# Optimization experiments

Measured on AMD Instinct MI355X. Metric: run time of the kernel, lower is better.

## Reference

```python
import jax, jax.numpy as jnp
import numpy as np

BN_EPS = 1e-5


def setup_inputs() -> dict:
    key = jax.random.key(0)
    k1, k2 = jax.random.split(key)
    B, P, S, D = 8, 64, 256, 256
    x = jax.random.normal(k1, (B, P, S, D), dtype=jnp.float32)
    # kaiming_normal_ on (planes, S, S): std = sqrt(2 / fan_in), fan_in = S*S
    std = np.sqrt(2.0 / (S * S)).astype(np.float32)
    weights = jax.random.normal(k2, (P, S, S), dtype=jnp.float32) * std
    gamma = jnp.ones((P,), dtype=jnp.float32)
    beta = jnp.zeros((P,), dtype=jnp.float32)
    return {"x": x, "weights": weights, "gamma": gamma, "beta": beta}


def reference(x, weights, gamma, beta):
    # x: (B, P, S, D); weights: (P, S, S)
    D = x.shape[-1]
    inv_dim = 1.0 / jnp.sqrt(jnp.asarray(D, dtype=x.dtype))
    # scores: (B, P, S, S) = x @ x^T / sqrt(D)
    scores = jnp.einsum('bpsd,bptd->bpst', x, x) * inv_dim
    # weighted reduction over last axis -> (B, P, S, 1)
    red = jnp.sum(scores * weights[None], axis=-1, keepdims=True)
    y = x + red  # residual broadcast over D
    # BatchNorm2d in training mode: per-channel batch stats over (B, S, D)
    mean = jnp.mean(y, axis=(0, 2, 3), keepdims=True)
    var = jnp.var(y, axis=(0, 2, 3), keepdims=True)
    y_hat = (y - mean) * jax.lax.rsqrt(var + BN_EPS)
    return y_hat * gamma[None, :, None, None] + beta[None, :, None, None]
```

## Files before the change

kernel.cpp:

```cpp
#include <hip/hip_runtime.h>

typedef __attribute__((ext_vector_type(8))) short short8;
typedef __attribute__((ext_vector_type(4))) float f32x4;

#define NB 8
#define NP 64
#define NS 256
#define ND 256
#define LSTR 264

__device__ __forceinline__ unsigned short f2bf(float f) {
    unsigned int u = __float_as_uint(f);
    u = (u + 0x7FFFu + ((u >> 16) & 1u)) >> 16;
    return (unsigned short)u;
}

__global__ __launch_bounds__(256) void k0_wt(
    const float* __restrict__ w, float* __restrict__ wt)
{
    const int o  = blockIdx.x * 256 + threadIdx.x;
    const int c  = o & 15;
    const int jb = (o >> 4) & 3;
    const int ps = o >> 6;
    const float* row = w + (size_t)ps * NS + 64 * jb + c;
    f32x4 v;
    v.x = row[0]; v.y = row[16]; v.z = row[32]; v.w = row[48];
    reinterpret_cast<f32x4*>(wt)[o] = v;
}

__global__ __launch_bounds__(1024, 4) void k1_gemm_red(
    const float* __restrict__ x, const float* __restrict__ wt,
    float* __restrict__ red, float* __restrict__ Sx, float* __restrict__ Sxx)
{
    __shared__ unsigned short Xl[NS * LSTR];
    __shared__ float red_l[4][NS];

    const int t    = threadIdx.x;
    const int lane = t & 63;
    const int wv   = t >> 6;
    const int ib   = wv >> 2;
    const int jb   = wv & 3;
    const int p    = blockIdx.x & 63;
    const int b    = blockIdx.x >> 6;

    const float* xb      = x + (size_t)(b * NP + p) * (NS * ND);
    const size_t rowbase = (size_t)(b * NP + p) * NS;

    #pragma unroll 4
    for (int i = 0; i < 16; ++i) {
        const int row = 16 * i + wv;
        f32x4 v = *reinterpret_cast<const f32x4*>(xb + row * ND + 4 * lane);
        float a = (v.x + v.y) + (v.z + v.w);
        #pragma unroll
        for (int off = 1; off < 64; off <<= 1) a += __shfl_xor(a, off, 64);
        if (lane == 0) Sx[rowbase + row] = a;
        unsigned long long pk =
              (unsigned long long)f2bf(v.x)
            | ((unsigned long long)f2bf(v.y) << 16)
            | ((unsigned long long)f2bf(v.z) << 32)
            | ((unsigned long long)f2bf(v.w) << 48);
        *reinterpret_cast<unsigned long long*>(&Xl[row * LSTR + 4 * lane]) = pk;
    }
    __syncthreads();

    const int qd = lane >> 4;
    const int c  = lane & 15;

    f32x4 acc[4][4] = {};
    #pragma unroll 2
    for (int k0 = 0; k0 < ND; k0 += 32) {
        const int kof = k0 + qd * 8;
        short8 afr[4], bfr[4];
        #pragma unroll
        for (int i = 0; i < 4; ++i)
            afr[i] = *reinterpret_cast<const short8*>(
                &Xl[(64 * ib + 16 * i + c) * LSTR + kof]);
        #pragma unroll
        for (int j = 0; j < 4; ++j)
            bfr[j] = *reinterpret_cast<const short8*>(
                &Xl[(64 * jb + 16 * j + c) * LSTR + kof]);
        #pragma unroll
        for (int i = 0; i < 4; ++i)
            #pragma unroll
            for (int j = 0; j < 4; ++j)
                acc[i][j] = __builtin_amdgcn_mfma_f32_16x16x32_bf16(
                    afr[i], bfr[j], acc[i][j], 0, 0, 0);
    }

    if (ib == jb && qd == (c >> 2)) {
        #pragma unroll
        for (int i = 0; i < 4; ++i)
            Sxx[rowbase + 64 * ib + 16 * i + c] = acc[i][i][c & 3];
    }

    const float* wtp = wt + (size_t)p * (NS * NS);
    #pragma unroll
    for (int i = 0; i < 4; ++i) {
        #pragma unroll
        for (int r = 0; r < 4; ++r) {
            const int rl = 16 * i + 4 * qd + r;
            const f32x4 wv = *reinterpret_cast<const f32x4*>(
                wtp + (size_t)(64 * ib + rl) * NS + 64 * jb + 4 * c);
            float s = acc[i][0][r] * wv.x + acc[i][1][r] * wv.y
                    + acc[i][2][r] * wv.z + acc[i][3][r] * wv.w;
            #pragma unroll
            for (int off = 1; off < 16; off <<= 1)
                s += __shfl_xor(s, off, 64);
            if (c == 0) red_l[jb][64 * ib + rl] = s;
        }
    }
    __syncthreads();
    if (t < NS)
        red[rowbase + t] =
            (red_l[0][t] + red_l[1][t] + red_l[2][t] + red_l[3][t]) * 0.0625f;
}

__global__ __launch_bounds__(256) void k2_stats(
    const float* __restrict__ red, const float* __restrict__ Sx,
    const float* __restrict__ Sxx, const float* __restrict__ gamma,
    const float* __restrict__ beta, float* __restrict__ sb)
{
    __shared__ float l1[256], l2[256];
    const int p = blockIdx.x;
    const int t = threadIdx.x;
    float sy = 0.f, syy = 0.f;
    for (int n = t; n < NB * NS; n += 256) {
        int bb = n >> 8, s = n & 255;
        size_t idx = (size_t)(bb * NP + p) * NS + s;
        float r = red[idx], a = Sx[idx], q = Sxx[idx];
        sy  += a + 256.f * r;
        syy += q + 2.f * r * a + 256.f * r * r;
    }
    l1[t] = sy; l2[t] = syy;
    __syncthreads();
    for (int off = 128; off > 0; off >>= 1) {
        if (t < off) { l1[t] += l1[t + off]; l2[t] += l2[t + off]; }
        __syncthreads();
    }
    if (t == 0) {
        const float invN = 1.f / (float)(NB * NS * ND);
        float mean = l1[0] * invN;
        float var  = l2[0] * invN - mean * mean;
        float sc   = gamma[p] * rsqrtf(var + 1e-5f);
        sb[p]      = sc;
        sb[64 + p] = beta[p] - mean * sc;
    }
}

__global__ __launch_bounds__(256) void k3_norm(
    const float* __restrict__ x, const float* __restrict__ red,
    const float* __restrict__ sb, float* __restrict__ out)
{
    const size_t f0 = (size_t)blockIdx.x * 1024 + threadIdx.x;
    #pragma unroll
    for (int k = 0; k < 4; ++k) {
        const size_t f = f0 + (size_t)k * 256;
        f32x4 v = reinterpret_cast<const f32x4*>(x)[f];
        const float r  = red[f >> 6];
        const int   pp = (int)((f >> 14) & 63);
        v = (v + r) * sb[pp] + sb[64 + pp];
        __builtin_nontemporal_store(v, reinterpret_cast<f32x4*>(out) + f);
    }
}

extern "C" void kernel_launch(void* const* d_in, const int* in_sizes, int n_in,
                              void* d_out, int out_size, void* d_ws, size_t ws_size,
                              hipStream_t stream)
{
    const float* x     = (const float*)d_in[0];
    const float* w     = (const float*)d_in[1];
    const float* gamma = (const float*)d_in[2];
    const float* beta  = (const float*)d_in[3];
    float* out = (float*)d_out;

    float* red = (float*)d_ws;
    float* Sx  = red + (size_t)NB * NP * NS;
    float* Sxx = Sx  + (size_t)NB * NP * NS;
    float* sb  = Sxx + (size_t)NB * NP * NS;

    float* wt = out;

    hipLaunchKernelGGL(k0_wt, dim3((NP * NS * NS) / (4 * 256)), dim3(256), 0, stream,
                       w, wt);
    hipLaunchKernelGGL(k1_gemm_red, dim3(NB * NP), dim3(1024), 0, stream,
                       x, wt, red, Sx, Sxx);
    hipLaunchKernelGGL(k2_stats, dim3(NP), dim3(256), 0, stream,
                       red, Sx, Sxx, gamma, beta, sb);
    hipLaunchKernelGGL(k3_norm, dim3((NB * NP * NS * ND) / (16 * 256)), dim3(256),
                       0, stream, x, red, sb, out);
}
```

Before: 297.3 us.

## Split GEMM K dimension across two blocks and combine partials in stats kernel

The score GEMM is split along the feature dimension into two halves, each handled by a separate 512-thread block with half-size LDS tile. This doubles the grid and halves LDS per block, which should raise occupancy and parallelism across CUs. Partial reductions, row sums and squared-norm diagonals are written per half and summed in the stats kernel, which also writes a combined red buffer for the normalize pass. The cost is extra workspace traffic, and each warp now handles two output tiles serially.

```diff
diff --git a/kernel.cpp b/kernel.cpp
--- a/kernel.cpp
+++ b/kernel.cpp
@@ -7,7 +7,9 @@
 #define NP 64
 #define NS 256
 #define ND 256
-#define LSTR 264
+#define KH 128
+#define LSTR 136
+#define NH (NB * NP * NS)
 
 __device__ __forceinline__ unsigned short f2bf(float f) {
     unsigned int u = __float_as_uint(f);
@@ -28,7 +30,7 @@
     reinterpret_cast<f32x4*>(wt)[o] = v;
 }
 
-__global__ __launch_bounds__(1024, 4) void k1_gemm_red(
+__global__ __launch_bounds__(512, 4) void k1_gemm_red(
     const float* __restrict__ x, const float* __restrict__ wt,
     float* __restrict__ red, float* __restrict__ Sx, float* __restrict__ Sxx)
 {
@@ -37,88 +39,98 @@
 
     const int t    = threadIdx.x;
     const int lane = t & 63;
-    const int wv   = t >> 6;
-    const int ib   = wv >> 2;
-    const int jb   = wv & 3;
-    const int p    = blockIdx.x & 63;
-    const int b    = blockIdx.x >> 6;
-
-    const float* xb      = x + (size_t)(b * NP + p) * (NS * ND);
+    const int wid  = t >> 6;
+    const int h    = blockIdx.x & 1;
+    const int p    = (blockIdx.x >> 1) & 63;
+    const int b    = blockIdx.x >> 7;
+
+    const float* xb      = x + (size_t)(b * NP + p) * (NS * ND) + h * KH;
     const size_t rowbase = (size_t)(b * NP + p) * NS;
+    const size_t hofs    = (size_t)h * NH;
+
+    const int l32 = lane & 31;
+    const int rup = lane >> 5;
 
     #pragma unroll 4
     for (int i = 0; i < 16; ++i) {
-        const int row = 16 * i + wv;
-        f32x4 v = *reinterpret_cast<const f32x4*>(xb + row * ND + 4 * lane);
+        const int row = 32 * wid + 2 * i + rup;
+        f32x4 v = *reinterpret_cast<const f32x4*>(xb + (size_t)row * ND + 4 * l32);
         float a = (v.x + v.y) + (v.z + v.w);
         #pragma unroll
-        for (int off = 1; off < 64; off <<= 1) a += __shfl_xor(a, off, 64);
-        if (lane == 0) Sx[rowbase + row] = a;
+        for (int off = 1; off < 32; off <<= 1) a += __shfl_xor(a, off, 64);
+        if (l32 == 0) Sx[hofs + rowbase + row] = a;
         unsigned long long pk =
               (unsigned long long)f2bf(v.x)
             | ((unsigned long long)f2bf(v.y) << 16)
             | ((unsigned long long)f2bf(v.z) << 32)
             | ((unsigned long long)f2bf(v.w) << 48);
-        *reinterpret_cast<unsigned long long*>(&Xl[row * LSTR + 4 * lane]) = pk;
+        *reinterpret_cast<unsigned long long*>(&Xl[row * LSTR + 4 * l32]) = pk;
     }
     __syncthreads();
 
     const int qd = lane >> 4;
     const int c  = lane & 15;
-
-    f32x4 acc[4][4] = {};
-    #pragma unroll 2
-    for (int k0 = 0; k0 < ND; k0 += 32) {
-        const int kof = k0 + qd * 8;
-        short8 afr[4], bfr[4];
+    const float* wtp = wt + (size_t)p * (NS * NS);
+
+    #pragma unroll 1
+    for (int tt = 0; tt < 2; ++tt) {
+        const int ib = (wid >> 2) + 2 * tt;
+        const int jb = wid & 3;
+
+        f32x4 acc[4][4] = {};
         #pragma unroll
-        for (int i = 0; i < 4; ++i)
-            afr[i] = *reinterpret_cast<const short8*>(
-                &Xl[(64 * ib + 16 * i + c) * LSTR + kof]);
+        for (int k0 = 0; k0 < KH; k0 += 32) {
+            const int kof = k0 + qd * 8;
+            short8 afr[4], bfr[4];
+            #pragma unroll
+            for (int i = 0; i < 4; ++i)
+                afr[i] = *reinterpret_cast<const short8*>(
+                    &Xl[(64 * ib + 16 * i + c) * LSTR + kof]);
+            #pragma unroll
+            for (int j = 0; j < 4; ++j)
+                bfr[j] = *reinterpret_cast<const short8*>(
+                    &Xl[(64 * jb + 16 * j + c) * LSTR + kof]);
+            #pragma unroll
+            for (int i = 0; i < 4; ++i)
+                #pragma unroll
+                for (int j = 0; j < 4; ++j)
+                    acc[i][j] = __builtin_amdgcn_mfma_f32_16x16x32_bf16(
+                        afr[i], bfr[j], acc[i][j], 0, 0, 0);
+        }
+
+        if (ib == jb && qd == (c >> 2)) {
+            #pragma unroll
+            for (int i = 0; i < 4; ++i)
+                Sxx[hofs + rowbase + 64 * ib + 16 * i + c] = acc[i][i][c & 3];
+        }
+
         #pragma unroll
-        for (int j = 0; j < 4; ++j)
-            bfr[j] = *reinterpret_cast<const short8*>(
-                &Xl[(64 * jb + 16 * j + c) * LSTR + kof]);
-        #pragma unroll
-        for (int i = 0; i < 4; ++i)
-            #pragma unroll
-            for (int j = 0; j < 4; ++j)
-                acc[i][j] = __builtin_amdgcn_mfma_f32_16x16x32_bf16(
-                    afr[i], bfr[j], acc[i][j], 0, 0, 0);
-    }
-
-    if (ib == jb && qd == (c >> 2)) {
-        #pragma unroll
-        for (int i = 0; i < 4; ++i)
-            Sxx[rowbase + 64 * ib + 16 * i + c] = acc[i][i][c & 3];
-    }
-
-    const float* wtp = wt + (size_t)p * (NS * NS);
-    #pragma unroll
-    for (int i = 0; i < 4; ++i) {
-        #pragma unroll
-        for (int r = 0; r < 4; ++r) {
-            const int rl = 16 * i + 4 * qd + r;
-            const f32x4 wv = *reinterpret_cast<const f32x4*>(
-                wtp + (size_t)(64 * ib + rl) * NS + 64 * jb + 4 * c);
-            float s = acc[i][0][r] * wv.x + acc[i][1][r] * wv.y
-                    + acc[i][2][r] * wv.z + acc[i][3][r] * wv.w;
-            #pragma unroll
-            for (int off = 1; off < 16; off <<= 1)
-                s += __shfl_xor(s, off, 64);
-            if (c == 0) red_l[jb][64 * ib + rl] = s;
+        for (int i = 0; i < 4; ++i) {
+            #pragma unroll
+            for (int r = 0; r < 4; ++r) {
+                const int rl = 16 * i + 4 * qd + r;
+                const f32x4 wvec = *reinterpret_cast<const f32x4*>(
+                    wtp + (size_t)(64 * ib + rl) * NS + 64 * jb + 4 * c);
+                float s = acc[i][0][r] * wvec.x + acc[i][1][r] * wvec.y
+                        + acc[i][2][r] * wvec.z + acc[i][3][r] * wvec.w;
+                #pragma unroll
+                for (int off = 1; off < 16; off <<= 1)
+                    s += __shfl_xor(s, off, 64);
+                if (c == 0) red_l[jb][64 * ib + rl] = s;
+            }
         }
     }
     __syncthreads();
     if (t < NS)
-        red[rowbase + t] =
+        red[hofs + rowbase + t] =
             (red_l[0][t] + red_l[1][t] + red_l[2][t] + red_l[3][t]) * 0.0625f;
 }
 
 __global__ __launch_bounds__(256) void k2_stats(
     const float* __restrict__ red, const float* __restrict__ Sx,
     const float* __restrict__ Sxx, const float* __restrict__ gamma,
-    const float* __restrict__ beta, float* __restrict__ sb)
+    const float* __restrict__ beta, float* __restrict__ sb,
+    float* __restrict__ redc)
 {
     __shared__ float l1[256], l2[256];
     const int p = blockIdx.x;
@@ -127,7 +139,10 @@
     for (int n = t; n < NB * NS; n += 256) {
         int bb = n >> 8, s = n & 255;
         size_t idx = (size_t)(bb * NP + p) * NS + s;
-        float r = red[idx], a = Sx[idx], q = Sxx[idx];
+        float r = red[idx] + red[NH + idx];
+        float a = Sx[idx]  + Sx[NH + idx];
+        float q = Sxx[idx] + Sxx[NH + idx];
+        redc[idx] = r;
         sy  += a + 256.f * r;
         syy += q + 2.f * r * a + 256.f * r * r;
     }
@@ -148,7 +163,7 @@
 }
 
 __global__ __launch_bounds__(256) void k3_norm(
-    const float* __restrict__ x, const float* __restrict__ red,
+    const float* __restrict__ x, const float* __restrict__ redc,
     const float* __restrict__ sb, float* __restrict__ out)
 {
     const size_t f0 = (size_t)blockIdx.x * 1024 + threadIdx.x;
@@ -156,7 +171,7 @@
     for (int k = 0; k < 4; ++k) {
         const size_t f = f0 + (size_t)k * 256;
         f32x4 v = reinterpret_cast<const f32x4*>(x)[f];
-        const float r  = red[f >> 6];
+        const float r  = redc[f >> 6];
         const int   pp = (int)((f >> 14) & 63);
         v = (v + r) * sb[pp] + sb[64 + pp];
         __builtin_nontemporal_store(v, reinterpret_cast<f32x4*>(out) + f);
@@ -173,19 +188,20 @@
     const float* beta  = (const float*)d_in[3];
     float* out = (float*)d_out;
 
-    float* red = (float*)d_ws;
-    float* Sx  = red + (size_t)NB * NP * NS;
-    float* Sxx = Sx  + (size_t)NB * NP * NS;
-    float* sb  = Sxx + (size_t)NB * NP * NS;
+    float* red  = (float*)d_ws;
+    float* Sx   = red  + 2 * (size_t)NH;
+    float* Sxx  = Sx   + 2 * (size_t)NH;
+    float* redc = Sxx  + 2 * (size_t)NH;
+    float* sb   = redc + (size_t)NH;
 
     float* wt = out;
 
     hipLaunchKernelGGL(k0_wt, dim3((NP * NS * NS) / (4 * 256)), dim3(256), 0, stream,
                        w, wt);
-    hipLaunchKernelGGL(k1_gemm_red, dim3(NB * NP), dim3(1024), 0, stream,
+    hipLaunchKernelGGL(k1_gemm_red, dim3(NB * NP * 2), dim3(512), 0, stream,
                        x, wt, red, Sx, Sxx);
     hipLaunchKernelGGL(k2_stats, dim3(NP), dim3(256), 0, stream,
-                       red, Sx, Sxx, gamma, beta, sb);
+                       red, Sx, Sxx, gamma, beta, sb, redc);
     hipLaunchKernelGGL(k3_norm, dim3((NB * NP * NS * ND) / (16 * 256)), dim3(256),
-                       0, stream, x, red, sb, out);
-}
+                       0, stream, x, redc, sb, out);
+}
```

Result: slower. 366.0 us (+23.1%).

## Pipeline x staging with MFMA GEMM over K chunks in gemm-reduce kernel

Applied to the files above, without the earlier changes.

Splits the load-convert-to-bf16 staging of each x slice into four 64-column chunks and runs the MFMA accumulation on completed chunks while the next chunk is being loaded. Row sums are accumulated per chunk and written after staging. This aims to hide global-load latency behind matrix-core work within the single large block per CU. The transposed weight scratch also moves from the output buffer into the workspace, which relies on the workspace being large enough.

```diff
diff --git a/kernel.cpp b/kernel.cpp
--- a/kernel.cpp
+++ b/kernel.cpp
@@ -46,46 +46,73 @@
     const float* xb      = x + (size_t)(b * NP + p) * (NS * ND);
     const size_t rowbase = (size_t)(b * NP + p) * NS;
 
-    #pragma unroll 4
-    for (int i = 0; i < 16; ++i) {
-        const int row = 16 * i + wv;
-        f32x4 v = *reinterpret_cast<const f32x4*>(xb + row * ND + 4 * lane);
-        float a = (v.x + v.y) + (v.z + v.w);
-        #pragma unroll
-        for (int off = 1; off < 64; off <<= 1) a += __shfl_xor(a, off, 64);
-        if (lane == 0) Sx[rowbase + row] = a;
-        unsigned long long pk =
-              (unsigned long long)f2bf(v.x)
-            | ((unsigned long long)f2bf(v.y) << 16)
-            | ((unsigned long long)f2bf(v.z) << 32)
-            | ((unsigned long long)f2bf(v.w) << 48);
-        *reinterpret_cast<unsigned long long*>(&Xl[row * LSTR + 4 * lane]) = pk;
-    }
-    __syncthreads();
-
-    const int qd = lane >> 4;
-    const int c  = lane & 15;
+    const int u   = lane >> 4;
+    const int l16 = lane & 15;
+
+    float a[4] = {0.f, 0.f, 0.f, 0.f};
 
     f32x4 acc[4][4] = {};
-    #pragma unroll 2
-    for (int k0 = 0; k0 < ND; k0 += 32) {
-        const int kof = k0 + qd * 8;
-        short8 afr[4], bfr[4];
-        #pragma unroll
-        for (int i = 0; i < 4; ++i)
-            afr[i] = *reinterpret_cast<const short8*>(
-                &Xl[(64 * ib + 16 * i + c) * LSTR + kof]);
+
+    auto STAGE = [&](int q) {
+        #pragma unroll
+        for (int j = 0; j < 4; ++j) {
+            const int row = 16 * (4 * j + u) + wv;
+            f32x4 v = *reinterpret_cast<const f32x4*>(
+                xb + (size_t)row * ND + 64 * q + 4 * l16);
+            float s = (v.x + v.y) + (v.z + v.w);
+            #pragma unroll
+            for (int off = 1; off < 16; off <<= 1) s += __shfl_xor(s, off, 64);
+            a[j] += s;
+            unsigned long long pk =
+                  (unsigned long long)f2bf(v.x)
+                | ((unsigned long long)f2bf(v.y) << 16)
+                | ((unsigned long long)f2bf(v.z) << 32)
+                | ((unsigned long long)f2bf(v.w) << 48);
+            *reinterpret_cast<unsigned long long*>(
+                &Xl[row * LSTR + 64 * q + 4 * l16]) = pk;
+        }
+    };
+
+    auto GEMM = [&](int g) {
+        #pragma unroll
+        for (int kk = 0; kk < 2; ++kk) {
+            const int kof = 64 * g + 32 * kk + u * 8;
+            short8 afr[4], bfr[4];
+            #pragma unroll
+            for (int i = 0; i < 4; ++i)
+                afr[i] = *reinterpret_cast<const short8*>(
+                    &Xl[(64 * ib + 16 * i + l16) * LSTR + kof]);
+            #pragma unroll
+            for (int j = 0; j < 4; ++j)
+                bfr[j] = *reinterpret_cast<const short8*>(
+                    &Xl[(64 * jb + 16 * j + l16) * LSTR + kof]);
+            #pragma unroll
+            for (int i = 0; i < 4; ++i)
+                #pragma unroll
+                for (int j = 0; j < 4; ++j)
+                    acc[i][j] = __builtin_amdgcn_mfma_f32_16x16x32_bf16(
+                        afr[i], bfr[j], acc[i][j], 0, 0, 0);
+        }
+    };
+
+    STAGE(0);
+    __syncthreads();
+    STAGE(1); GEMM(0);
+    __syncthreads();
+    STAGE(2); GEMM(1);
+    __syncthreads();
+    STAGE(3);
+    if (l16 == 0) {
         #pragma unroll
         for (int j = 0; j < 4; ++j)
-            bfr[j] = *reinterpret_cast<const short8*>(
-                &Xl[(64 * jb + 16 * j + c) * LSTR + kof]);
-        #pragma unroll
-        for (int i = 0; i < 4; ++i)
-            #pragma unroll
-            for (int j = 0; j < 4; ++j)
-                acc[i][j] = __builtin_amdgcn_mfma_f32_16x16x32_bf16(
-                    afr[i], bfr[j], acc[i][j], 0, 0, 0);
-    }
+            Sx[rowbase + 16 * (4 * j + u) + wv] = a[j];
+    }
+    GEMM(2);
+    __syncthreads();
+    GEMM(3);
+
+    const int qd = u;
+    const int c  = l16;
 
     if (ib == jb && qd == (c >> 2)) {
         #pragma unroll
@@ -99,10 +126,10 @@
         #pragma unroll
         for (int r = 0; r < 4; ++r) {
             const int rl = 16 * i + 4 * qd + r;
-            const f32x4 wv = *reinterpret_cast<const f32x4*>(
+            const f32x4 wvec = *reinterpret_cast<const f32x4*>(
                 wtp + (size_t)(64 * ib + rl) * NS + 64 * jb + 4 * c);
-            float s = acc[i][0][r] * wv.x + acc[i][1][r] * wv.y
-                    + acc[i][2][r] * wv.z + acc[i][3][r] * wv.w;
+            float s = acc[i][0][r] * wvec.x + acc[i][1][r] * wvec.y
+                    + acc[i][2][r] * wvec.z + acc[i][3][r] * wvec.w;
             #pragma unroll
             for (int off = 1; off < 16; off <<= 1)
                 s += __shfl_xor(s, off, 64);
@@ -127,9 +154,9 @@
     for (int n = t; n < NB * NS; n += 256) {
         int bb = n >> 8, s = n & 255;
         size_t idx = (size_t)(bb * NP + p) * NS + s;
-        float r = red[idx], a = Sx[idx], q = Sxx[idx];
-        sy  += a + 256.f * r;
-        syy += q + 2.f * r * a + 256.f * r * r;
+        float r = red[idx], aa = Sx[idx], q = Sxx[idx];
+        sy  += aa + 256.f * r;
+        syy += q + 2.f * r * aa + 256.f * r * r;
     }
     l1[t] = sy; l2[t] = syy;
     __syncthreads();
@@ -177,8 +204,7 @@
     float* Sx  = red + (size_t)NB * NP * NS;
     float* Sxx = Sx  + (size_t)NB * NP * NS;
     float* sb  = Sxx + (size_t)NB * NP * NS;
-
-    float* wt = out;
+    float* wt  = sb + 128;
 
     hipLaunchKernelGGL(k0_wt, dim3((NP * NS * NS) / (4 * 256)), dim3(256), 0, stream,
                        w, wt);
```

New measurement: 321.2 us. 8.0% more time.
